# Kernel optimization log

Measured on AMD Instinct MI355X. Metric: run time of the kernel, lower is better.

Reference implementation:

```python
import jax, jax.numpy as jnp
import numpy as np

W = 128      # window_size
BACK = 1     # look_backward
FWD = 0      # look_forward (causal)


def _look_around(x, backward=BACK, forward=FWD, pad_value=-1):
    t = x.shape[1]
    pads = [(0, 0), (backward, forward)] + [(0, 0)] * (x.ndim - 2)
    p = jnp.pad(x, pads, constant_values=pad_value)
    return jnp.concatenate([p[:, i:i + t] for i in range(forward + backward + 1)], axis=2)


def setup_inputs() -> dict:
    key = jax.random.key(0)
    kq, kk, kv = jax.random.split(key, 3)
    B, H, T, D = 4, 8, 8192, 64
    q = jax.random.normal(kq, (B, H, T, D), jnp.float32)
    k = jax.random.normal(kk, (B, H, T, D), jnp.float32)
    v = jax.random.normal(kv, (B, H, T, D), jnp.float32)
    return {"q": q, "k": k, "v": v}


def reference(q, k, v):
    B, H, T, D = q.shape
    win = T // W
    # flatten batch/head, split into windows
    bq = q.reshape(B * H, win, W, D)
    bk = k.reshape(B * H, win, W, D)
    bv = v.reshape(B * H, win, W, D)
    bk = _look_around(bk)
    bv = _look_around(bv)

    bq_t = jnp.arange(T, dtype=jnp.int32).reshape(1, win, W)       # query positions
    bq_k = _look_around(bq_t, pad_value=-1)                        # key positions (pad = -1)

    scale = D ** -0.5
    dots = jnp.einsum('bwid,bwjd->bwij', bq, bk) * scale
    mask_value = -jnp.finfo(dots.dtype).max

    causal_mask = bq_t[:, :, :, None] < bq_k[:, :, None, :]
    pad_mask = (bq_k == -1)[:, :, None, :]
    dots = jnp.where(causal_mask | pad_mask, mask_value, dots)

    attn = jax.nn.softmax(dots, axis=-1)
    out = jnp.einsum('bwij,bwjd->bwid', attn, bv)
    return out.reshape(B, H, T, D)
```

## Files before the change

kernel.cpp:

```cpp
#include <hip/hip_runtime.h>
#include <hip/hip_bf16.h>

typedef __bf16 bf16x8 __attribute__((ext_vector_type(8)));
typedef float  f32x4  __attribute__((ext_vector_type(4)));
typedef float  f32x16 __attribute__((ext_vector_type(16)));
typedef unsigned int u32x4 __attribute__((ext_vector_type(4)));

#define TQ 8192
#define DD 64

static __device__ __forceinline__ unsigned cvtpk(float a, float b) {
    unsigned r;
    asm("v_cvt_pk_bf16_f32 %0, %1, %2" : "=v"(r) : "v"(a), "v"(b));
    return r;
}

__global__ __launch_bounds__(256, 3)
void lattn_kernel(const float* __restrict__ q, const float* __restrict__ k,
                  const float* __restrict__ v, float* __restrict__ out)
{
    const int bx0  = blockIdx.x;
    const int bx   = ((bx0 & 7) << 8) | (bx0 >> 3);
    const int bh   = bx >> 6;
    const int w    = bx & 63;
    const int tid  = threadIdx.x;
    const int lane = tid & 63;
    const int wv   = tid >> 6;
    const int l31  = lane & 31;
    const int hi   = lane >> 5;

    const size_t base  = ((size_t)bh * TQ + w * 128) * DD;
    const int    krow0 = w * 128 - 128;

    const int kb0   = (w == 0) ? 4 : 0;
    const int kbend = wv + 4;

    const float* kbase = k + ((size_t)bh * TQ + krow0) * DD + hi * 8;
    const float* vbase = v + ((size_t)bh * TQ + krow0) * DD;

    f32x4 kn[8];
    {
        const float* kp = kbase + (size_t)(kb0 * 32 + l31) * DD;
        #pragma unroll
        for (int s = 0; s < 4; ++s) {
            kn[2 * s]     = *(const f32x4*)(kp + 16 * s);
            kn[2 * s + 1] = *(const f32x4*)(kp + 16 * s + 4);
        }
    }

    const float SCL = 0.18033688011112042f;
    bf16x8 qf[4];
    {
        const float* qp = q + base + (size_t)(wv * 32 + l31) * DD + hi * 8;
        #pragma unroll
        for (int s = 0; s < 4; ++s) {
            f32x4 a = *(const f32x4*)(qp + 16 * s);
            f32x4 b = *(const f32x4*)(qp + 16 * s + 4);
            u32x4 t;
            t[0] = cvtpk(a[0] * SCL, a[1] * SCL);
            t[1] = cvtpk(a[2] * SCL, a[3] * SCL);
            t[2] = cvtpk(b[0] * SCL, b[1] * SCL);
            t[3] = cvtpk(b[2] * SCL, b[3] * SCL);
            qf[s] = __builtin_bit_cast(bf16x8, t);
        }
    }

    bf16x8 kf[4];
    #pragma unroll
    for (int s = 0; s < 4; ++s) {
        u32x4 t;
        t[0] = cvtpk(kn[2 * s][0],     kn[2 * s][1]);
        t[1] = cvtpk(kn[2 * s][2],     kn[2 * s][3]);
        t[2] = cvtpk(kn[2 * s + 1][0], kn[2 * s + 1][1]);
        t[3] = cvtpk(kn[2 * s + 1][2], kn[2 * s + 1][3]);
        kf[s] = __builtin_bit_cast(bf16x8, t);
    }

    f32x16 o0 = {}, o1 = {};
    float lsum = 0.f;

    for (int kb = kb0; kb <= kbend; ++kb) {
        float vn[32];
        {
            const float* vp = vbase + (size_t)(kb * 32 + hi * 8) * DD + l31;
            #pragma unroll
            for (int s2 = 0; s2 < 2; ++s2) {
                #pragma unroll
                for (int e = 0; e < 8; ++e) {
                    vn[s2 * 8 + e]      = vp[(s2 * 16 + e) * DD];
                    vn[16 + s2 * 8 + e] = vp[(s2 * 16 + e) * DD + 32];
                }
            }
        }
        if (kb < kbend) {
            const float* kp = kbase + (size_t)((kb + 1) * 32 + l31) * DD;
            #pragma unroll
            for (int s = 0; s < 4; ++s) {
                kn[2 * s]     = *(const f32x4*)(kp + 16 * s);
                kn[2 * s + 1] = *(const f32x4*)(kp + 16 * s + 4);
            }
        }

        f32x16 sacc = {};
        __builtin_amdgcn_s_setprio(1);
        #pragma unroll
        for (int s = 0; s < 4; ++s)
            sacc = __builtin_amdgcn_mfma_f32_32x32x16_bf16(kf[s], qf[s], sacc, 0, 0, 0);
        __builtin_amdgcn_s_setprio(0);

        float p[16];
        float ts = 0.f;
        if (kb == kbend) {
            #pragma unroll
            for (int r = 0; r < 16; ++r) {
                float sv = sacc[r];
                int jj = (r & 3) + 8 * (r >> 2) + 4 * hi;
                if (jj > l31) sv = -3.0e38f;
                float e = exp2f(sv);
                p[r] = e;
                ts += e;
            }
        } else {
            #pragma unroll
            for (int r = 0; r < 16; ++r) {
                float e = exp2f(sacc[r]);
                p[r] = e;
                ts += e;
            }
        }
        ts += __shfl_xor(ts, 32, 64);
        lsum += ts;

        unsigned pk[8], xw[8];
        #pragma unroll
        for (int m = 0; m < 8; ++m) pk[m] = cvtpk(p[2 * m], p[2 * m + 1]);
        #pragma unroll
        for (int m = 0; m < 8; ++m) xw[m] = (unsigned)__shfl_xor((int)pk[m], 32, 64);
        u32x4 f0, f1;
        f0[0] = hi ? xw[2] : pk[0]; f0[1] = hi ? xw[3] : pk[1];
        f0[2] = hi ? pk[2] : xw[0]; f0[3] = hi ? pk[3] : xw[1];
        f1[0] = hi ? xw[6] : pk[4]; f1[1] = hi ? xw[7] : pk[5];
        f1[2] = hi ? pk[6] : xw[4]; f1[3] = hi ? pk[7] : xw[5];
        bf16x8 pf0 = __builtin_bit_cast(bf16x8, f0);
        bf16x8 pf1 = __builtin_bit_cast(bf16x8, f1);

        u32x4 w00, w01, w10, w11;
        #pragma unroll
        for (int m = 0; m < 4; ++m) {
            w00[m] = cvtpk(vn[2 * m],      vn[2 * m + 1]);
            w01[m] = cvtpk(vn[8 + 2 * m],  vn[9 + 2 * m]);
            w10[m] = cvtpk(vn[16 + 2 * m], vn[17 + 2 * m]);
            w11[m] = cvtpk(vn[24 + 2 * m], vn[25 + 2 * m]);
        }
        bf16x8 vb00 = __builtin_bit_cast(bf16x8, w00);
        bf16x8 vb01 = __builtin_bit_cast(bf16x8, w01);
        bf16x8 vb10 = __builtin_bit_cast(bf16x8, w10);
        bf16x8 vb11 = __builtin_bit_cast(bf16x8, w11);

        __builtin_amdgcn_s_setprio(1);
        o0 = __builtin_amdgcn_mfma_f32_32x32x16_bf16(pf0, vb00, o0, 0, 0, 0);
        o0 = __builtin_amdgcn_mfma_f32_32x32x16_bf16(pf1, vb01, o0, 0, 0, 0);
        o1 = __builtin_amdgcn_mfma_f32_32x32x16_bf16(pf0, vb10, o1, 0, 0, 0);
        o1 = __builtin_amdgcn_mfma_f32_32x32x16_bf16(pf1, vb11, o1, 0, 0, 0);
        __builtin_amdgcn_s_setprio(0);

        if (kb < kbend) {
            #pragma unroll
            for (int s = 0; s < 4; ++s) {
                u32x4 t;
                t[0] = cvtpk(kn[2 * s][0],     kn[2 * s][1]);
                t[1] = cvtpk(kn[2 * s][2],     kn[2 * s][3]);
                t[2] = cvtpk(kn[2 * s + 1][0], kn[2 * s + 1][1]);
                t[3] = cvtpk(kn[2 * s + 1][2], kn[2 * s + 1][3]);
                kf[s] = __builtin_bit_cast(bf16x8, t);
            }
        }
    }

    const float rinv = 1.0f / lsum;
    #pragma unroll
    for (int r = 0; r < 16; ++r) {
        int rowr = (r & 3) + 8 * (r >> 2) + 4 * hi;
        float rl = __shfl(rinv, rowr, 64);
        float* op = out + base + (size_t)(wv * 32 + rowr) * DD;
        op[l31]      = o0[r] * rl;
        op[l31 + 32] = o1[r] * rl;
    }
}

extern "C" void kernel_launch(void* const* d_in, const int* in_sizes, int n_in,
                              void* d_out, int out_size, void* d_ws, size_t ws_size,
                              hipStream_t stream) {
    const float* q = (const float*)d_in[0];
    const float* k = (const float*)d_in[1];
    const float* v = (const float*)d_in[2];
    float* out = (float*)d_out;
    dim3 grid(32 * 64);
    dim3 block(256);
    lattn_kernel<<<grid, block, 0, stream>>>(q, k, v, out);
}
```

Before: 84.47 us.

## Stage V tiles through LDS with async global_load_lds double buffering

V is no longer loaded with 32 scalar strided global loads per lane. Each 32-row V block is now copied into a per-wave double-buffered LDS region with 16-byte global_load_lds DMA, prefetched one block ahead and guarded by manual vmcnt waits. The goal is coalesced V traffic and overlap of the V fetch with the QK MFMA and softmax. In exchange it uses 64KB of LDS per block and lowers launch bounds occupancy from 3 to 2, and it relies on hand-counted vmcnt values being correct.

```diff
diff --git a/kernel.cpp b/kernel.cpp
--- a/kernel.cpp
+++ b/kernel.cpp
@@ -14,11 +14,20 @@
     asm("v_cvt_pk_bf16_f32 %0, %1, %2" : "=v"(r) : "v"(a), "v"(b));
     return r;
 }
-
-__global__ __launch_bounds__(256, 3)
+#define SB() __builtin_amdgcn_sched_barrier(0)
+
+static __device__ __forceinline__ void dma16(const float* g, float* l) {
+    __builtin_amdgcn_global_load_lds(
+        (const __attribute__((address_space(1))) void*)g,
+        (__attribute__((address_space(3))) void*)l, 16, 0, 0);
+}
+
+__global__ __launch_bounds__(256, 2)
 void lattn_kernel(const float* __restrict__ q, const float* __restrict__ k,
                   const float* __restrict__ v, float* __restrict__ out)
 {
+    __shared__ float Vlds[4][2][2048];
+
     const int bx0  = blockIdx.x;
     const int bx   = ((bx0 & 7) << 8) | (bx0 >> 3);
     const int bh   = bx >> 6;
@@ -38,15 +47,8 @@
     const float* kbase = k + ((size_t)bh * TQ + krow0) * DD + hi * 8;
     const float* vbase = v + ((size_t)bh * TQ + krow0) * DD;
 
-    f32x4 kn[8];
-    {
-        const float* kp = kbase + (size_t)(kb0 * 32 + l31) * DD;
-        #pragma unroll
-        for (int s = 0; s < 4; ++s) {
-            kn[2 * s]     = *(const f32x4*)(kp + 16 * s);
-            kn[2 * s + 1] = *(const f32x4*)(kp + 16 * s + 4);
-        }
-    }
+    const int jr   = lane >> 4;
+    const int dcol = (lane & 15) * 4;
 
     const float SCL = 0.18033688011112042f;
     bf16x8 qf[4];
@@ -65,6 +67,21 @@
         }
     }
 
+    f32x4 kn[8];
+    {
+        const float* kp = kbase + (size_t)(kb0 * 32 + l31) * DD;
+        #pragma unroll
+        for (int s = 0; s < 4; ++s) {
+            kn[2 * s]     = *(const f32x4*)(kp + 16 * s);
+            kn[2 * s + 1] = *(const f32x4*)(kp + 16 * s + 4);
+        }
+    }
+    SB();
+    #pragma unroll
+    for (int c = 0; c < 8; ++c)
+        dma16(vbase + (size_t)(kb0 * 32 + c * 4 + jr) * DD + dcol,
+              &Vlds[wv][kb0 & 1][c * 256]);
+    SB();
     bf16x8 kf[4];
     #pragma unroll
     for (int s = 0; s < 4; ++s) {
@@ -80,25 +97,20 @@
     float lsum = 0.f;
 
     for (int kb = kb0; kb <= kbend; ++kb) {
-        float vn[32];
-        {
-            const float* vp = vbase + (size_t)(kb * 32 + hi * 8) * DD + l31;
-            #pragma unroll
-            for (int s2 = 0; s2 < 2; ++s2) {
-                #pragma unroll
-                for (int e = 0; e < 8; ++e) {
-                    vn[s2 * 8 + e]      = vp[(s2 * 16 + e) * DD];
-                    vn[16 + s2 * 8 + e] = vp[(s2 * 16 + e) * DD + 32];
-                }
-            }
-        }
-        if (kb < kbend) {
+        const bool more = (kb < kbend);
+        if (more) {
             const float* kp = kbase + (size_t)((kb + 1) * 32 + l31) * DD;
             #pragma unroll
             for (int s = 0; s < 4; ++s) {
                 kn[2 * s]     = *(const f32x4*)(kp + 16 * s);
                 kn[2 * s + 1] = *(const f32x4*)(kp + 16 * s + 4);
             }
+            SB();
+            #pragma unroll
+            for (int c = 0; c < 8; ++c)
+                dma16(vbase + (size_t)((kb + 1) * 32 + c * 4 + jr) * DD + dcol,
+                      &Vlds[wv][(kb + 1) & 1][c * 256]);
+            SB();
         }
 
         f32x16 sacc = {};
@@ -117,16 +129,11 @@
                 int jj = (r & 3) + 8 * (r >> 2) + 4 * hi;
                 if (jj > l31) sv = -3.0e38f;
                 float e = exp2f(sv);
-                p[r] = e;
-                ts += e;
+                p[r] = e; ts += e;
             }
         } else {
             #pragma unroll
-            for (int r = 0; r < 16; ++r) {
-                float e = exp2f(sacc[r]);
-                p[r] = e;
-                ts += e;
-            }
+            for (int r = 0; r < 16; ++r) { float e = exp2f(sacc[r]); p[r] = e; ts += e; }
         }
         ts += __shfl_xor(ts, 32, 64);
         lsum += ts;
@@ -144,13 +151,18 @@
         bf16x8 pf0 = __builtin_bit_cast(bf16x8, f0);
         bf16x8 pf1 = __builtin_bit_cast(bf16x8, f1);
 
+        if (more) { asm volatile("s_waitcnt vmcnt(16)" ::: "memory"); }
+        else      { asm volatile("s_waitcnt vmcnt(0)"  ::: "memory"); }
+        SB();
+
+        const float* vp = &Vlds[wv][kb & 1][0] + hi * 512 + l31;
         u32x4 w00, w01, w10, w11;
         #pragma unroll
         for (int m = 0; m < 4; ++m) {
-            w00[m] = cvtpk(vn[2 * m],      vn[2 * m + 1]);
-            w01[m] = cvtpk(vn[8 + 2 * m],  vn[9 + 2 * m]);
-            w10[m] = cvtpk(vn[16 + 2 * m], vn[17 + 2 * m]);
-            w11[m] = cvtpk(vn[24 + 2 * m], vn[25 + 2 * m]);
+            w00[m] = cvtpk(vp[(2 * m) * 64],           vp[(2 * m + 1) * 64]);
+            w01[m] = cvtpk(vp[(2 * m + 16) * 64],      vp[(2 * m + 17) * 64]);
+            w10[m] = cvtpk(vp[(2 * m) * 64 + 32],      vp[(2 * m + 1) * 64 + 32]);
+            w11[m] = cvtpk(vp[(2 * m + 16) * 64 + 32], vp[(2 * m + 17) * 64 + 32]);
         }
         bf16x8 vb00 = __builtin_bit_cast(bf16x8, w00);
         bf16x8 vb01 = __builtin_bit_cast(bf16x8, w01);
@@ -164,7 +176,7 @@
         o1 = __builtin_amdgcn_mfma_f32_32x32x16_bf16(pf1, vb11, o1, 0, 0, 0);
         __builtin_amdgcn_s_setprio(0);
 
-        if (kb < kbend) {
+        if (more) {
             #pragma unroll
             for (int s = 0; s < 4; ++s) {
                 u32x4 t;
```

Result: faster. 82.05 us (-2.9%).
